# Performance work log

Measured on AMD Instinct MI355X. Metric: run time of the kernel, lower is better.

The kernel has to match this reference:

```python
import jax, jax.numpy as jnp
import numpy as np

N = 100000   # total atoms in the batch
E = 400000   # directed edges (bonds both directions)
F = 11       # raw atom feature dim (Linear(11, vector_dim))
D = 512      # vector_dim
L = 5        # num_conv_layers
G = 2048     # number of molecules (graphs) in the batch


def setup_inputs() -> dict:
    key = jax.random.key(0)
    k = jax.random.split(key, 6)
    x = jax.random.uniform(k[0], (N, F), dtype=jnp.float32)  # nonneg counts-like features
    edge_index = jax.random.randint(k[1], (2, E), 0, N, dtype=jnp.int32)
    batch = jnp.sort(jax.random.randint(k[2], (N,), 0, G, dtype=jnp.int32))
    exp_W = jax.random.normal(k[3], (F, D), dtype=jnp.float32) * (1.0 / np.sqrt(F))
    exp_b = jnp.zeros((D,), dtype=jnp.float32)
    gcn_W = jax.random.normal(k[4], (L, D, D), dtype=jnp.float32) * (1.0 / np.sqrt(D))
    gcn_b = jnp.zeros((L, D), dtype=jnp.float32)
    return {"x": x, "edge_index": edge_index, "batch": batch,
            "exp_W": exp_W, "exp_b": exp_b, "gcn_W": gcn_W, "gcn_b": gcn_b}


def reference(x, edge_index, batch, exp_W, exp_b, gcn_W, gcn_b):
    # GraphEmbedding.forward (eval mode: dropout = identity)
    src, dst = edge_index[0], edge_index[1]
    h = jnp.log(x + 1.0) @ exp_W + exp_b  # expansion Linear(11, D)  -> [N, D]

    # GCN normalization with improved=True: self-loop weight 2.0
    # deg_i = sum of incoming edge weights (1.0) + 2.0 self-loop
    ones_e = jnp.ones((E,), dtype=h.dtype)
    deg = jax.ops.segment_sum(ones_e, dst, num_segments=N) + 2.0
    dinv = jax.lax.rsqrt(deg)              # deg >= 2, always finite
    enorm = dinv[src] * dinv[dst]          # per-edge norm (weight 1.0)
    self_norm = 2.0 * dinv * dinv          # self-loop norm (weight 2.0)

    for l in range(L):
        xw = h @ gcn_W[l]                                   # [N, D]
        msg = enorm[:, None] * xw[src]                      # gather + scale, [E, D]
        agg = jax.ops.segment_sum(msg, dst, num_segments=N)  # scatter-add
        agg = agg + self_norm[:, None] * xw + gcn_b[l]
        h = h + jax.nn.relu(agg)                            # residual + relu (dropout off)

    # global_add_pool over molecules
    return jax.ops.segment_sum(h, batch, num_segments=G)    # [G, D]
```

## Files before the change

kernel.cpp:

```cpp
#include <hip/hip_runtime.h>
#include <hip/hip_bf16.h>
#include <stdint.h>

typedef __attribute__((ext_vector_type(8))) short bf16x8;
typedef __attribute__((ext_vector_type(4))) float f32x4;
typedef unsigned short ushort_t;
typedef unsigned int uint_t;

__device__ __forceinline__ unsigned short f2bf(float f) {
  unsigned u = __float_as_uint(f);
  u += 0x7fffu + ((u >> 16) & 1u);
  return (unsigned short)(u >> 16);
}
__device__ __forceinline__ float bf2f(unsigned u16) {
  return __uint_as_float(u16 << 16);
}
__device__ __forceinline__ void fma8(float* a, uint4 u, float w) {
  a[0] += w * bf2f(u.x & 0xffffu); a[1] += w * bf2f(u.x >> 16);
  a[2] += w * bf2f(u.y & 0xffffu); a[3] += w * bf2f(u.y >> 16);
  a[4] += w * bf2f(u.z & 0xffffu); a[5] += w * bf2f(u.z >> 16);
  a[6] += w * bf2f(u.w & 0xffffu); a[7] += w * bf2f(u.w >> 16);
}
__device__ __forceinline__ bf16x8 pack8(const float* a) {
  union { bf16x8 v; ushort_t s[8]; } u;
#pragma unroll
  for (int j = 0; j < 8; ++j) u.s[j] = f2bf(a[j]);
  return u.v;
}

__global__ void k_zero(int* __restrict__ p, int n) {
  int i = blockIdx.x * blockDim.x + threadIdx.x;
  if (i < n) p[i] = 0;
}

__global__ void k_prep_w(const float* __restrict__ W, ushort_t* __restrict__ Wt, int total) {
  int idx = blockIdx.x * blockDim.x + threadIdx.x;
  if (idx >= total) return;
  int j   = idx & 7;
  int col = (idx >> 3) & 511;
  int kg  = (idx >> 12) & 3;
  int kt  = (idx >> 14) & 15;
  int l   = idx >> 18;
  int k = kt * 32 + kg * 8 + j;
  Wt[idx] = f2bf(W[((size_t)(l * 512 + k)) * 512 + col]);
}

__global__ __launch_bounds__(256) void k_expand(const float* __restrict__ x,
                                                const float* __restrict__ eW,
                                                const float* __restrict__ eb,
                                                ushort_t* __restrict__ h, int N) {
  const int wid = (blockIdx.x * 256 + threadIdx.x) >> 6;
  const int nw = (gridDim.x * 256) >> 6;
  const int l = threadIdx.x & 63;

  float wf[11][8];
  float bias[8];
#pragma unroll
  for (int f = 0; f < 11; ++f) {
    float4 a = *(const float4*)&eW[f * 512 + l * 8];
    float4 b = *(const float4*)&eW[f * 512 + l * 8 + 4];
    wf[f][0] = a.x; wf[f][1] = a.y; wf[f][2] = a.z; wf[f][3] = a.w;
    wf[f][4] = b.x; wf[f][5] = b.y; wf[f][6] = b.z; wf[f][7] = b.w;
  }
  {
    float4 a = *(const float4*)&eb[l * 8];
    float4 b = *(const float4*)&eb[l * 8 + 4];
    bias[0] = a.x; bias[1] = a.y; bias[2] = a.z; bias[3] = a.w;
    bias[4] = b.x; bias[5] = b.y; bias[6] = b.z; bias[7] = b.w;
  }

  for (int n = wid; n < N; n += nw) {
    float xv = (l < 11) ? x[(size_t)n * 11 + l] : 0.f;
    float lx = log1pf(xv);
    float acc[8];
#pragma unroll
    for (int j = 0; j < 8; ++j) acc[j] = bias[j];
#pragma unroll
    for (int f = 0; f < 11; ++f) {
      float c = __shfl(lx, f, 64);
#pragma unroll
      for (int j = 0; j < 8; ++j) acc[j] += c * wf[f][j];
    }
    uint4 pu;
    pu.x = (uint_t)f2bf(acc[0]) | ((uint_t)f2bf(acc[1]) << 16);
    pu.y = (uint_t)f2bf(acc[2]) | ((uint_t)f2bf(acc[3]) << 16);
    pu.z = (uint_t)f2bf(acc[4]) | ((uint_t)f2bf(acc[5]) << 16);
    pu.w = (uint_t)f2bf(acc[6]) | ((uint_t)f2bf(acc[7]) << 16);
    *(uint4*)(h + (size_t)n * 512 + l * 8) = pu;
  }
}

__global__ void k_deg(const int* __restrict__ dst, int* __restrict__ deg, int E) {
  int e = blockIdx.x * blockDim.x + threadIdx.x;
  if (e < E) atomicAdd(&deg[dst[e]], 1);
}

__global__ void k_dinv(const int* __restrict__ deg, float* __restrict__ dinv,
                       float* __restrict__ selfn, int N) {
  int n = blockIdx.x * blockDim.x + threadIdx.x;
  if (n >= N) return;
  float d = (float)deg[n] + 2.0f;
  dinv[n] = rsqrtf(d);
  selfn[n] = 2.0f / d;
}

__global__ void k_scan_a(const int* __restrict__ deg, int* __restrict__ off,
                         int* __restrict__ bsum, int N) {
  __shared__ int sd[256];
  int t = threadIdx.x;
  int i0 = blockIdx.x * 1024 + t * 4;
  int d[4];
#pragma unroll
  for (int j = 0; j < 4; ++j) d[j] = (i0 + j < N) ? deg[i0 + j] : 0;
  int ts = d[0] + d[1] + d[2] + d[3];
  sd[t] = ts;
  __syncthreads();
  for (int o = 1; o < 256; o <<= 1) {
    int v = (t >= o) ? sd[t - o] : 0;
    __syncthreads();
    sd[t] += v;
    __syncthreads();
  }
  int incl = sd[t];
  int run = incl - ts;
#pragma unroll
  for (int j = 0; j < 4; ++j) {
    if (i0 + j < N) off[i0 + j] = run;
    run += d[j];
  }
  if (t == 255) bsum[blockIdx.x] = incl;
}

__global__ void k_scan_b(const int* __restrict__ bsum, int* __restrict__ bpre, int nb,
                         int* __restrict__ off, int N, int E) {
  __shared__ int sd[256];
  int t = threadIdx.x;
  int v = (t < nb) ? bsum[t] : 0;
  sd[t] = v;
  __syncthreads();
  for (int o = 1; o < 256; o <<= 1) {
    int u = (t >= o) ? sd[t - o] : 0;
    __syncthreads();
    sd[t] += u;
    __syncthreads();
  }
  if (t < nb) bpre[t] = sd[t] - v;
  if (t == 0) off[N] = E;
}

__global__ void k_scan_c(int* __restrict__ off, const int* __restrict__ bpre, int N) {
  int i = blockIdx.x * blockDim.x + threadIdx.x;
  if (i < N) off[i] += bpre[i >> 10];
}

__global__ void k_fill(const int* __restrict__ src, const int* __restrict__ dst,
                       const int* __restrict__ off, int* __restrict__ cur,
                       int* __restrict__ ssrc, int E) {
  int e = blockIdx.x * blockDim.x + threadIdx.x;
  if (e >= E) return;
  int t = dst[e];
  int p = atomicAdd(&cur[t], 1);
  ssrc[off[t] + p] = src[e];
}

__global__ __launch_bounds__(1024, 4) void k_fused(const ushort_t* __restrict__ hin,
                                                   ushort_t* __restrict__ hout,
                                                   const ushort_t* __restrict__ Wt,
                                                   const float* __restrict__ gbl,
                                                   const int* __restrict__ off,
                                                   const int* __restrict__ ssrc,
                                                   const float* __restrict__ dinv,
                                                   const float* __restrict__ selfn, int N) {
  __shared__ alignas(16) ushort_t s_tile[64 * 512];
  __shared__ alignas(16) ushort_t Bbuf[2][16384];
  const int t = threadIdx.x;
  const int wv = t >> 6, ln = t & 63;
  const int bm0 = blockIdx.x * 64;

  {
    const ushort_t* src = Wt + wv * 1024 + ln * 8;
    __builtin_amdgcn_global_load_lds(
        (const __attribute__((address_space(1))) uint_t*)src,
        (__attribute__((address_space(3))) uint_t*)&Bbuf[0][wv * 1024], 16, 0, 0);
    __builtin_amdgcn_global_load_lds(
        (const __attribute__((address_space(1))) uint_t*)(src + 512),
        (__attribute__((address_space(3))) uint_t*)&Bbuf[0][wv * 1024 + 512], 16, 0, 0);
  }

#pragma unroll
  for (int pr = 0; pr < 2; ++pr) {
    int r0l = wv * 4 + pr * 2, r1l = r0l + 1;
    int r0 = bm0 + r0l, r1 = bm0 + r1l;
    bool v0 = r0 < N, v1 = r1 < N;
    float a0[8], a1[8];
#pragma unroll
    for (int j = 0; j < 8; ++j) { a0[j] = 0.f; a1[j] = 0.f; }
    int i0 = 0, e0 = 0, i1 = 0, e1 = 0;
    float dn0 = 0.f, dn1 = 0.f;
    if (v0) {
      i0 = off[r0]; e0 = off[r0 + 1]; dn0 = dinv[r0];
      uint4 u = *(const uint4*)(hin + (size_t)r0 * 512 + ln * 8);
      fma8(a0, u, selfn[r0]);
    }
    if (v1) {
      i1 = off[r1]; e1 = off[r1 + 1]; dn1 = dinv[r1];
      uint4 u = *(const uint4*)(hin + (size_t)r1 * 512 + ln * 8);
      fma8(a1, u, selfn[r1]);
    }
    while (i0 < e0 && i1 < e1) {
      int n0 = ssrc[i0++], n1 = ssrc[i1++];
      float w0 = dn0 * dinv[n0], w1 = dn1 * dinv[n1];
      uint4 u0 = *(const uint4*)(hin + (size_t)n0 * 512 + ln * 8);
      uint4 u1 = *(const uint4*)(hin + (size_t)n1 * 512 + ln * 8);
      fma8(a0, u0, w0);
      fma8(a1, u1, w1);
    }
    while (i0 < e0) {
      int n0 = ssrc[i0++];
      float w0 = dn0 * dinv[n0];
      uint4 u0 = *(const uint4*)(hin + (size_t)n0 * 512 + ln * 8);
      fma8(a0, u0, w0);
    }
    while (i1 < e1) {
      int n1 = ssrc[i1++];
      float w1 = dn1 * dinv[n1];
      uint4 u1 = *(const uint4*)(hin + (size_t)n1 * 512 + ln * 8);
      fma8(a1, u1, w1);
    }
    *(bf16x8*)((char*)s_tile + r0l * 1024 + ((ln * 16) ^ ((r0l & 7) << 4))) = pack8(a0);
    *(bf16x8*)((char*)s_tile + r1l * 1024 + ((ln * 16) ^ ((r1l & 7) << 4))) = pack8(a1);
  }
  __syncthreads();

  const int wrow = wv >> 3, wcol = wv & 7;
  const int l15 = ln & 15, l4 = ln >> 4;
  f32x4 acc[2][4];
#pragma unroll
  for (int i = 0; i < 2; ++i)
#pragma unroll
    for (int j = 0; j < 4; ++j) acc[i][j] = (f32x4){0.f, 0.f, 0.f, 0.f};

  for (int kt = 0; kt < 16; ++kt) {
    const int cur = kt & 1;
    if (kt < 15) {
      const ushort_t* src = Wt + (kt + 1) * 16384 + wv * 1024 + ln * 8;
      __builtin_amdgcn_global_load_lds(
          (const __attribute__((address_space(1))) uint_t*)src,
          (__attribute__((address_space(3))) uint_t*)&Bbuf[cur ^ 1][wv * 1024], 16, 0, 0);
      __builtin_amdgcn_global_load_lds(
          (const __attribute__((address_space(1))) uint_t*)(src + 512),
          (__attribute__((address_space(3))) uint_t*)&Bbuf[cur ^ 1][wv * 1024 + 512], 16, 0, 0);
    }
    bf16x8 a[2], b[4];
#pragma unroll
    for (int i = 0; i < 2; ++i) {
      int row = wrow * 32 + i * 16 + l15;
      a[i] = *(const bf16x8*)((const char*)s_tile + row * 1024 +
                              (((kt * 64 + l4 * 16)) ^ ((row & 7) << 4)));
    }
#pragma unroll
    for (int j = 0; j < 4; ++j)
      b[j] = *(const bf16x8*)&Bbuf[cur][l4 * 4096 + (wcol * 64 + j * 16 + l15) * 8];
#pragma unroll
    for (int i = 0; i < 2; ++i)
#pragma unroll
      for (int j = 0; j < 4; ++j)
        acc[i][j] = __builtin_amdgcn_mfma_f32_16x16x32_bf16(a[i], b[j], acc[i][j], 0, 0, 0);
    __syncthreads();
  }

  float* cst = (float*)&Bbuf[0][0];
#pragma unroll
  for (int p = 0; p < 2; ++p) {
    if (wrow == p) {
#pragma unroll
      for (int i = 0; i < 2; ++i)
#pragma unroll
        for (int v = 0; v < 4; ++v) {
          int r32 = i * 16 + l4 * 4 + v;
#pragma unroll
          for (int j = 0; j < 4; ++j)
            cst[r32 * 512 + wcol * 64 + j * 16 + l15] = acc[i][j][v];
        }
    }
    __syncthreads();
#pragma unroll
    for (int w = 0; w < 2; ++w) {
      int g = t + w * 1024;
      int row_l = g >> 6, colg = g & 63;
      int grow = bm0 + p * 32 + row_l;
      if (grow < N) {
        float c[8];
        float4 c0 = *(const float4*)&cst[row_l * 512 + colg * 8];
        float4 c1 = *(const float4*)&cst[row_l * 512 + colg * 8 + 4];
        c[0] = c0.x; c[1] = c0.y; c[2] = c0.z; c[3] = c0.w;
        c[4] = c1.x; c[5] = c1.y; c[6] = c1.z; c[7] = c1.w;
        float4 b0 = *(const float4*)&gbl[colg * 8];
        float4 b1 = *(const float4*)&gbl[colg * 8 + 4];
        float bb[8] = {b0.x, b0.y, b0.z, b0.w, b1.x, b1.y, b1.z, b1.w};
        uint4 hu = *(const uint4*)(hin + (size_t)grow * 512 + colg * 8);
        float hv[8];
        hv[0] = bf2f(hu.x & 0xffffu); hv[1] = bf2f(hu.x >> 16);
        hv[2] = bf2f(hu.y & 0xffffu); hv[3] = bf2f(hu.y >> 16);
        hv[4] = bf2f(hu.z & 0xffffu); hv[5] = bf2f(hu.z >> 16);
        hv[6] = bf2f(hu.w & 0xffffu); hv[7] = bf2f(hu.w >> 16);
#pragma unroll
        for (int j = 0; j < 8; ++j) hv[j] += fmaxf(c[j] + bb[j], 0.f);
        uint4 pu;
        pu.x = (uint_t)f2bf(hv[0]) | ((uint_t)f2bf(hv[1]) << 16);
        pu.y = (uint_t)f2bf(hv[2]) | ((uint_t)f2bf(hv[3]) << 16);
        pu.z = (uint_t)f2bf(hv[4]) | ((uint_t)f2bf(hv[5]) << 16);
        pu.w = (uint_t)f2bf(hv[6]) | ((uint_t)f2bf(hv[7]) << 16);
        *(uint4*)(hout + (size_t)grow * 512 + colg * 8) = pu;
      }
    }
    __syncthreads();
  }
}

__device__ __forceinline__ int lbound(const int* a, int n, int v) {
  int lo = 0, hi = n;
  while (lo < hi) {
    int m = (lo + hi) >> 1;
    if (a[m] < v) lo = m + 1; else hi = m;
  }
  return lo;
}

__global__ __launch_bounds__(256) void k_pool(const ushort_t* __restrict__ h,
                                              const int* __restrict__ batch,
                                              float* __restrict__ out, int N) {
  __shared__ float red[4 * 512];
  int g = blockIdx.x;
  int t = threadIdx.x;
  int w = t >> 6, l = t & 63;
  int start = lbound(batch, N, g);
  int end = lbound(batch, N, g + 1);
  float acc[8];
#pragma unroll
  for (int j = 0; j < 8; ++j) acc[j] = 0.f;
  for (int n = start + w; n < end; n += 4) {
    uint4 u = *(const uint4*)(h + (size_t)n * 512 + l * 8);
    acc[0] += bf2f(u.x & 0xffffu); acc[1] += bf2f(u.x >> 16);
    acc[2] += bf2f(u.y & 0xffffu); acc[3] += bf2f(u.y >> 16);
    acc[4] += bf2f(u.z & 0xffffu); acc[5] += bf2f(u.z >> 16);
    acc[6] += bf2f(u.w & 0xffffu); acc[7] += bf2f(u.w >> 16);
  }
#pragma unroll
  for (int j = 0; j < 8; ++j) red[w * 512 + l * 8 + j] = acc[j];
  __syncthreads();
  if (t < 128) {
    float4 sv = make_float4(0.f, 0.f, 0.f, 0.f);
#pragma unroll
    for (int ww = 0; ww < 4; ++ww) {
      float4 v = *(const float4*)&red[ww * 512 + t * 4];
      sv.x += v.x; sv.y += v.y; sv.z += v.z; sv.w += v.w;
    }
    *(float4*)&out[(size_t)g * 512 + t * 4] = sv;
  }
}

extern "C" void kernel_launch(void* const* d_in, const int* in_sizes, int n_in,
                              void* d_out, int out_size, void* d_ws, size_t ws_size,
                              hipStream_t stream) {
  const float* x  = (const float*)d_in[0];
  const int* ei   = (const int*)d_in[1];
  const int* batch= (const int*)d_in[2];
  const float* eW = (const float*)d_in[3];
  const float* eb = (const float*)d_in[4];
  const float* gW = (const float*)d_in[5];
  const float* gb = (const float*)d_in[6];
  float* out = (float*)d_out;

  const int N = in_sizes[0] / 11;
  const int E = in_sizes[1] / 2;
  const int G = out_size / 512;
  const int L = in_sizes[5] / (512 * 512);

  const int* src = ei;
  const int* dst = ei + E;

  size_t nd = (size_t)N * 512;
  char* p = (char*)d_ws;
  auto carve = [&](size_t bytes) {
    char* q = p;
    p += (bytes + 255) & ~(size_t)255;
    return q;
  };
  ushort_t* h0        = (ushort_t*)carve(nd * 2);
  ushort_t* h1        = (ushort_t*)carve(nd * 2);
  ushort_t* Wt        = (ushort_t*)carve((size_t)L * 512 * 512 * 2);
  int* deg            = (int*)carve((size_t)N * 4);
  float* dinv         = (float*)carve((size_t)N * 4);
  float* selfn        = (float*)carve((size_t)N * 4);
  int* off            = (int*)carve(((size_t)N + 1) * 4);
  int* cur            = (int*)carve((size_t)N * 4);
  int* ssrc           = (int*)carve((size_t)E * 4);
  int* bsum           = (int*)carve(1024);
  int* bpre           = (int*)carve(1024);

  k_zero<<<(N + 255) / 256, 256, 0, stream>>>(deg, N);
  k_zero<<<(N + 255) / 256, 256, 0, stream>>>(cur, N);

  int totW = L * 512 * 512;
  k_prep_w<<<(totW + 255) / 256, 256, 0, stream>>>(gW, Wt, totW);
  k_expand<<<2048, 256, 0, stream>>>(x, eW, eb, h0, N);
  k_deg<<<(E + 255) / 256, 256, 0, stream>>>(dst, deg, E);
  k_dinv<<<(N + 255) / 256, 256, 0, stream>>>(deg, dinv, selfn, N);
  int nb = (N + 1023) / 1024;
  k_scan_a<<<nb, 256, 0, stream>>>(deg, off, bsum, N);
  k_scan_b<<<1, 256, 0, stream>>>(bsum, bpre, nb, off, N, E);
  k_scan_c<<<(N + 255) / 256, 256, 0, stream>>>(off, bpre, N);
  k_fill<<<(E + 255) / 256, 256, 0, stream>>>(src, dst, off, cur, ssrc, E);

  ushort_t* hb[2] = {h0, h1};
  dim3 fgrid((N + 63) / 64);
  for (int l = 0; l < L; ++l) {
    k_fused<<<fgrid, 1024, 0, stream>>>(hb[l & 1], hb[(l & 1) ^ 1],
                                        Wt + (size_t)l * 512 * 512,
                                        gb + (size_t)l * 512,
                                        off, ssrc, dinv, selfn, N);
  }
  k_pool<<<G, 256, 0, stream>>>(hb[L & 1], batch, out, N);
}
```

Baseline: 1.124 ms.

## Split fused gather-GEMM layer kernel into separate aggregation and GEMM kernels

Each GCN layer's fused kernel is replaced by two kernels. A wave-per-node, grid-stride aggregation kernel writes the normalized neighbour sum to a pre-swizzled bf16 buffer using nontemporal stores. A GEMM kernel then bulk-loads that tile into LDS and applies the weight, bias, relu and residual in place on a single h buffer. The aim is to stop the latency-bound irregular gather from stalling the large-LDS, low-occupancy MFMA kernel, at the cost of an extra global write and read of an N×512 intermediate per layer.

```diff
diff --git a/kernel.cpp b/kernel.cpp
--- a/kernel.cpp
+++ b/kernel.cpp
@@ -4,6 +4,7 @@
 
 typedef __attribute__((ext_vector_type(8))) short bf16x8;
 typedef __attribute__((ext_vector_type(4))) float f32x4;
+typedef __attribute__((ext_vector_type(4))) unsigned int u32x4;
 typedef unsigned short ushort_t;
 typedef unsigned int uint_t;
 
@@ -21,11 +22,9 @@
   a[4] += w * bf2f(u.z & 0xffffu); a[5] += w * bf2f(u.z >> 16);
   a[6] += w * bf2f(u.w & 0xffffu); a[7] += w * bf2f(u.w >> 16);
 }
-__device__ __forceinline__ bf16x8 pack8(const float* a) {
-  union { bf16x8 v; ushort_t s[8]; } u;
-#pragma unroll
-  for (int j = 0; j < 8; ++j) u.s[j] = f2bf(a[j]);
-  return u.v;
+__device__ __forceinline__ void nt_store16(void* p, uint_t x, uint_t y, uint_t z, uint_t w) {
+  u32x4 v; v.x = x; v.y = y; v.z = z; v.w = w;
+  __builtin_nontemporal_store(v, (u32x4*)p);
 }
 
 __global__ void k_zero(int* __restrict__ p, int n) {
@@ -163,14 +162,47 @@
   ssrc[off[t] + p] = src[e];
 }
 
-__global__ __launch_bounds__(1024, 4) void k_fused(const ushort_t* __restrict__ hin,
-                                                   ushort_t* __restrict__ hout,
-                                                   const ushort_t* __restrict__ Wt,
-                                                   const float* __restrict__ gbl,
-                                                   const int* __restrict__ off,
-                                                   const int* __restrict__ ssrc,
-                                                   const float* __restrict__ dinv,
-                                                   const float* __restrict__ selfn, int N) {
+__global__ __launch_bounds__(256) void k_agg2s(const ushort_t* __restrict__ h,
+                                               ushort_t* __restrict__ s,
+                                               const int* __restrict__ off,
+                                               const int* __restrict__ ssrc,
+                                               const float* __restrict__ dinv,
+                                               const float* __restrict__ selfn, int N) {
+  const int wid = (blockIdx.x * 256 + threadIdx.x) >> 6;
+  const int nw = (gridDim.x * 256) >> 6;
+  const int l = threadIdx.x & 63;
+
+  for (int n = wid; n < N; n += nw) {
+    int s0 = off[n], s1 = off[n + 1];
+    float dn = dinv[n];
+    float acc[8];
+    {
+      uint4 u = *(const uint4*)(h + (size_t)n * 512 + l * 8);
+      float sn = selfn[n];
+      acc[0] = sn * bf2f(u.x & 0xffffu); acc[1] = sn * bf2f(u.x >> 16);
+      acc[2] = sn * bf2f(u.y & 0xffffu); acc[3] = sn * bf2f(u.y >> 16);
+      acc[4] = sn * bf2f(u.z & 0xffffu); acc[5] = sn * bf2f(u.z >> 16);
+      acc[6] = sn * bf2f(u.w & 0xffffu); acc[7] = sn * bf2f(u.w >> 16);
+    }
+    for (int i = s0; i < s1; ++i) {
+      int sv = ssrc[i];
+      float w = dn * dinv[sv];
+      uint4 u = *(const uint4*)(h + (size_t)sv * 512 + l * 8);
+      fma8(acc, u, w);
+    }
+    char* dstp = (char*)s + (size_t)n * 1024 + ((l * 16) ^ ((n & 7) << 4));
+    nt_store16(dstp,
+               (uint_t)f2bf(acc[0]) | ((uint_t)f2bf(acc[1]) << 16),
+               (uint_t)f2bf(acc[2]) | ((uint_t)f2bf(acc[3]) << 16),
+               (uint_t)f2bf(acc[4]) | ((uint_t)f2bf(acc[5]) << 16),
+               (uint_t)f2bf(acc[6]) | ((uint_t)f2bf(acc[7]) << 16));
+  }
+}
+
+__global__ __launch_bounds__(1024, 4) void k_gemm64(const ushort_t* __restrict__ s,
+                                                    const ushort_t* __restrict__ Wt,
+                                                    const float* __restrict__ gbl,
+                                                    ushort_t* __restrict__ h, int N) {
   __shared__ alignas(16) ushort_t s_tile[64 * 512];
   __shared__ alignas(16) ushort_t Bbuf[2][16384];
   const int t = threadIdx.x;
@@ -178,57 +210,24 @@
   const int bm0 = blockIdx.x * 64;
 
   {
-    const ushort_t* src = Wt + wv * 1024 + ln * 8;
+    const ushort_t* sbase = s + (size_t)bm0 * 512;
+#pragma unroll
+    for (int r = 0; r < 4; ++r) {
+      const ushort_t* srcp = sbase + (((r * 16 + wv) * 64 + ln) << 3);
+      __builtin_amdgcn_global_load_lds(
+          (const __attribute__((address_space(1))) uint_t*)srcp,
+          (__attribute__((address_space(3))) uint_t*)&s_tile[((r * 16 + wv) * 64) << 3],
+          16, 0, 0);
+    }
+  }
+  {
+    const ushort_t* srcp = Wt + wv * 1024 + ln * 8;
     __builtin_amdgcn_global_load_lds(
-        (const __attribute__((address_space(1))) uint_t*)src,
+        (const __attribute__((address_space(1))) uint_t*)srcp,
         (__attribute__((address_space(3))) uint_t*)&Bbuf[0][wv * 1024], 16, 0, 0);
     __builtin_amdgcn_global_load_lds(
-        (const __attribute__((address_space(1))) uint_t*)(src + 512),
+        (const __attribute__((address_space(1))) uint_t*)(srcp + 512),
         (__attribute__((address_space(3))) uint_t*)&Bbuf[0][wv * 1024 + 512], 16, 0, 0);
-  }
-
-#pragma unroll
-  for (int pr = 0; pr < 2; ++pr) {
-    int r0l = wv * 4 + pr * 2, r1l = r0l + 1;
-    int r0 = bm0 + r0l, r1 = bm0 + r1l;
-    bool v0 = r0 < N, v1 = r1 < N;
-    float a0[8], a1[8];
-#pragma unroll
-    for (int j = 0; j < 8; ++j) { a0[j] = 0.f; a1[j] = 0.f; }
-    int i0 = 0, e0 = 0, i1 = 0, e1 = 0;
-    float dn0 = 0.f, dn1 = 0.f;
-    if (v0) {
-      i0 = off[r0]; e0 = off[r0 + 1]; dn0 = dinv[r0];
-      uint4 u = *(const uint4*)(hin + (size_t)r0 * 512 + ln * 8);
-      fma8(a0, u, selfn[r0]);
-    }
-    if (v1) {
-      i1 = off[r1]; e1 = off[r1 + 1]; dn1 = dinv[r1];
-      uint4 u = *(const uint4*)(hin + (size_t)r1 * 512 + ln * 8);
-      fma8(a1, u, selfn[r1]);
-    }
-    while (i0 < e0 && i1 < e1) {
-      int n0 = ssrc[i0++], n1 = ssrc[i1++];
-      float w0 = dn0 * dinv[n0], w1 = dn1 * dinv[n1];
-      uint4 u0 = *(const uint4*)(hin + (size_t)n0 * 512 + ln * 8);
-      uint4 u1 = *(const uint4*)(hin + (size_t)n1 * 512 + ln * 8);
-      fma8(a0, u0, w0);
-      fma8(a1, u1, w1);
-    }
-    while (i0 < e0) {
-      int n0 = ssrc[i0++];
-      float w0 = dn0 * dinv[n0];
-      uint4 u0 = *(const uint4*)(hin + (size_t)n0 * 512 + ln * 8);
-      fma8(a0, u0, w0);
-    }
-    while (i1 < e1) {
-      int n1 = ssrc[i1++];
-      float w1 = dn1 * dinv[n1];
-      uint4 u1 = *(const uint4*)(hin + (size_t)n1 * 512 + ln * 8);
-      fma8(a1, u1, w1);
-    }
-    *(bf16x8*)((char*)s_tile + r0l * 1024 + ((ln * 16) ^ ((r0l & 7) << 4))) = pack8(a0);
-    *(bf16x8*)((char*)s_tile + r1l * 1024 + ((ln * 16) ^ ((r1l & 7) << 4))) = pack8(a1);
   }
   __syncthreads();
 
@@ -243,12 +242,12 @@
   for (int kt = 0; kt < 16; ++kt) {
     const int cur = kt & 1;
     if (kt < 15) {
-      const ushort_t* src = Wt + (kt + 1) * 16384 + wv * 1024 + ln * 8;
+      const ushort_t* srcp = Wt + (kt + 1) * 16384 + wv * 1024 + ln * 8;
       __builtin_amdgcn_global_load_lds(
-          (const __attribute__((address_space(1))) uint_t*)src,
+          (const __attribute__((address_space(1))) uint_t*)srcp,
           (__attribute__((address_space(3))) uint_t*)&Bbuf[cur ^ 1][wv * 1024], 16, 0, 0);
       __builtin_amdgcn_global_load_lds(
-          (const __attribute__((address_space(1))) uint_t*)(src + 512),
+          (const __attribute__((address_space(1))) uint_t*)(srcp + 512),
           (__attribute__((address_space(3))) uint_t*)&Bbuf[cur ^ 1][wv * 1024 + 512], 16, 0, 0);
     }
     bf16x8 a[2], b[4];
@@ -256,7 +255,7 @@
     for (int i = 0; i < 2; ++i) {
       int row = wrow * 32 + i * 16 + l15;
       a[i] = *(const bf16x8*)((const char*)s_tile + row * 1024 +
-                              (((kt * 64 + l4 * 16)) ^ ((row & 7) << 4)));
+                              ((kt * 64 + l4 * 16) ^ ((row & 7) << 4)));
     }
 #pragma unroll
     for (int j = 0; j < 4; ++j)
@@ -290,15 +289,13 @@
       int row_l = g >> 6, colg = g & 63;
       int grow = bm0 + p * 32 + row_l;
       if (grow < N) {
-        float c[8];
         float4 c0 = *(const float4*)&cst[row_l * 512 + colg * 8];
         float4 c1 = *(const float4*)&cst[row_l * 512 + colg * 8 + 4];
-        c[0] = c0.x; c[1] = c0.y; c[2] = c0.z; c[3] = c0.w;
-        c[4] = c1.x; c[5] = c1.y; c[6] = c1.z; c[7] = c1.w;
+        float c[8] = {c0.x, c0.y, c0.z, c0.w, c1.x, c1.y, c1.z, c1.w};
         float4 b0 = *(const float4*)&gbl[colg * 8];
         float4 b1 = *(const float4*)&gbl[colg * 8 + 4];
         float bb[8] = {b0.x, b0.y, b0.z, b0.w, b1.x, b1.y, b1.z, b1.w};
-        uint4 hu = *(const uint4*)(hin + (size_t)grow * 512 + colg * 8);
+        uint4 hu = *(const uint4*)(h + (size_t)grow * 512 + colg * 8);
         float hv[8];
         hv[0] = bf2f(hu.x & 0xffffu); hv[1] = bf2f(hu.x >> 16);
         hv[2] = bf2f(hu.y & 0xffffu); hv[3] = bf2f(hu.y >> 16);
@@ -311,7 +308,7 @@
         pu.y = (uint_t)f2bf(hv[2]) | ((uint_t)f2bf(hv[3]) << 16);
         pu.z = (uint_t)f2bf(hv[4]) | ((uint_t)f2bf(hv[5]) << 16);
         pu.w = (uint_t)f2bf(hv[6]) | ((uint_t)f2bf(hv[7]) << 16);
-        *(uint4*)(hout + (size_t)grow * 512 + colg * 8) = pu;
+        *(uint4*)(h + (size_t)grow * 512 + colg * 8) = pu;
       }
     }
     __syncthreads();
@@ -380,15 +377,15 @@
   const int* src = ei;
   const int* dst = ei + E;
 
-  size_t nd = (size_t)N * 512;
+  const int Npad = (N + 63) & ~63;
   char* p = (char*)d_ws;
   auto carve = [&](size_t bytes) {
     char* q = p;
     p += (bytes + 255) & ~(size_t)255;
     return q;
   };
-  ushort_t* h0        = (ushort_t*)carve(nd * 2);
-  ushort_t* h1        = (ushort_t*)carve(nd * 2);
+  ushort_t* h         = (ushort_t*)carve((size_t)N * 512 * 2);
+  ushort_t* s         = (ushort_t*)carve((size_t)Npad * 512 * 2);
   ushort_t* Wt        = (ushort_t*)carve((size_t)L * 512 * 512 * 2);
   int* deg            = (int*)carve((size_t)N * 4);
   float* dinv         = (float*)carve((size_t)N * 4);
@@ -404,7 +401,7 @@
 
   int totW = L * 512 * 512;
   k_prep_w<<<(totW + 255) / 256, 256, 0, stream>>>(gW, Wt, totW);
-  k_expand<<<2048, 256, 0, stream>>>(x, eW, eb, h0, N);
+  k_expand<<<2048, 256, 0, stream>>>(x, eW, eb, h, N);
   k_deg<<<(E + 255) / 256, 256, 0, stream>>>(dst, deg, E);
   k_dinv<<<(N + 255) / 256, 256, 0, stream>>>(deg, dinv, selfn, N);
   int nb = (N + 1023) / 1024;
@@ -413,13 +410,11 @@
   k_scan_c<<<(N + 255) / 256, 256, 0, stream>>>(off, bpre, N);
   k_fill<<<(E + 255) / 256, 256, 0, stream>>>(src, dst, off, cur, ssrc, E);
 
-  ushort_t* hb[2] = {h0, h1};
-  dim3 fgrid((N + 63) / 64);
+  dim3 ggrid((N + 63) / 64);
   for (int l = 0; l < L; ++l) {
-    k_fused<<<fgrid, 1024, 0, stream>>>(hb[l & 1], hb[(l & 1) ^ 1],
-                                        Wt + (size_t)l * 512 * 512,
-                                        gb + (size_t)l * 512,
-                                        off, ssrc, dinv, selfn, N);
-  }
-  k_pool<<<G, 256, 0, stream>>>(hb[L & 1], batch, out, N);
-}
+    k_agg2s<<<2048, 256, 0, stream>>>(h, s, off, ssrc, dinv, selfn, N);
+    k_gemm64<<<ggrid, 1024, 0, stream>>>(s, Wt + (size_t)l * 512 * 512,
+                                         gb + (size_t)l * 512, h, N);
+  }
+  k_pool<<<G, 256, 0, stream>>>(h, batch, out, N);
+}
```

Result: slower. 1.213 ms (+7.9%).
